# Kernel tuning notes

Hardware: AMD Instinct MI355X
Metric: run time of the kernel (lower is better)

The kernel has to match this reference:

```python
import jax, jax.numpy as jnp
import numpy as np

B, N, D, H = 4, 8192, 1024, 8
HD = D // H  # 128
EPS = 1e-5


def setup_inputs() -> dict:
    key = jax.random.key(0)
    k1, k2, k3 = jax.random.split(key, 3)
    x = jax.random.normal(k1, (B, N, D), dtype=jnp.float32)
    mask = jax.random.randint(k2, (B, 1, N), 0, 2).astype(jnp.bool_)
    # nn.Linear(dim, 3*dim, bias=False): weight [3D, D]; store as [D, 3D] for x @ w
    w_qkv = jax.random.normal(k3, (D, 3 * D), dtype=jnp.float32) / np.sqrt(D)
    gamma = jnp.ones((D,), dtype=jnp.float32)
    beta = jnp.zeros((D,), dtype=jnp.float32)
    return {"x": x, "mask": mask, "w_qkv": w_qkv, "gamma": gamma, "beta": beta}


def _layernorm(x, gamma, beta):
    mu = jnp.mean(x, axis=-1, keepdims=True)
    var = jnp.mean(jnp.square(x - mu), axis=-1, keepdims=True)
    return (x - mu) * jax.lax.rsqrt(var + EPS) * gamma + beta


def reference(x, mask, w_qkv, gamma, beta):
    xn = _layernorm(x, gamma, beta)                       # [B,N,D]
    qkv = xn @ w_qkv                                      # [B,N,3D]
    q, k, v = jnp.split(qkv, 3, axis=-1)
    # 'b n (h d) -> b h n d'
    def to_heads(t):
        return t.reshape(B, N, H, HD).transpose(0, 2, 1, 3)
    q, k, v = to_heads(q), to_heads(k), to_heads(v)       # [B,H,N,HD]
    q = jax.nn.sigmoid(q)
    k = jnp.tanh(k)
    k = jnp.where(mask[..., None], 0.0, k)                # masked_fill -> 0
    kv = jnp.einsum('bhnd,bhne->bhde', k, v)              # k^T @ v, [B,H,HD,HD]
    out = jnp.einsum('bhnd,bhde->bhne', q, kv)            # [B,H,N,HD]
    out = out.transpose(0, 2, 1, 3).reshape(B, N, D)      # 'b h n d -> b n (h d)'
    return out  # output_layer='None' -> Identity
```

## Files before the change

### kernel.cpp

```cpp
#include <hip/hip_runtime.h>

#define EPS 1e-5f
#define B_ 4
#define N_ 8192
#define D_ 1024
#define H_ 8
#define HD_ 128
#define M_TOT 32768
#define NQKV 3072

typedef __bf16 bf16x8 __attribute__((ext_vector_type(8)));
typedef float f32x4 __attribute__((ext_vector_type(4)));

__device__ __forceinline__ float bf2f(unsigned short u) {
    unsigned int v = ((unsigned int)u) << 16;
    return __uint_as_float(v);
}
__device__ __forceinline__ unsigned short f2bf(float f) {
    unsigned int u = __float_as_uint(f);
    u += 0x7fffu + ((u >> 16) & 1u);
    return (unsigned short)(u >> 16);
}

__device__ __forceinline__ float fast_sigmoid(float v) {
    return __builtin_amdgcn_rcpf(1.0f + __expf(-v));
}
__device__ __forceinline__ float fast_tanh(float v) {
    return 1.0f - 2.0f * __builtin_amdgcn_rcpf(1.0f + __expf(2.0f * v));
}

__device__ __forceinline__ void gl_lds16(const void* g, void* l) {
    __builtin_amdgcn_global_load_lds(
        (const __attribute__((address_space(1))) unsigned int*)g,
        (__attribute__((address_space(3))) unsigned int*)l, 16, 0, 0);
}

__global__ __launch_bounds__(256) void ln_kernel(const float* __restrict__ x,
                                                 const float* __restrict__ gamma,
                                                 const float* __restrict__ beta,
                                                 unsigned short* __restrict__ xn) {
    const int row = blockIdx.x;
    const int t = threadIdx.x;
    const float* xr = x + (size_t)row * D_;
    float4 xv = ((const float4*)xr)[t];
    float s = xv.x + xv.y + xv.z + xv.w;
    float s2 = xv.x * xv.x + xv.y * xv.y + xv.z * xv.z + xv.w * xv.w;
    for (int off = 32; off > 0; off >>= 1) {
        s += __shfl_down(s, off);
        s2 += __shfl_down(s2, off);
    }
    __shared__ float red[8];
    if ((t & 63) == 0) { red[t >> 6] = s; red[4 + (t >> 6)] = s2; }
    __syncthreads();
    float ts = red[0] + red[1] + red[2] + red[3];
    float ts2 = red[4] + red[5] + red[6] + red[7];
    float mu = ts * (1.0f / D_);
    float var = ts2 * (1.0f / D_) - mu * mu;
    float rs = rsqrtf(var + EPS);
    float4 g = ((const float4*)gamma)[t];
    float4 bt = ((const float4*)beta)[t];
    ushort4 o;
    o.x = f2bf((xv.x - mu) * rs * g.x + bt.x);
    o.y = f2bf((xv.y - mu) * rs * g.y + bt.y);
    o.z = f2bf((xv.z - mu) * rs * g.z + bt.z);
    o.w = f2bf((xv.w - mu) * rs * g.w + bt.w);
    ((ushort4*)(xn + (size_t)row * D_))[t] = o;
}

__global__ __launch_bounds__(256) void wt_kernel(const float* __restrict__ w,
                                                 unsigned short* __restrict__ wT) {
    __shared__ float tile[64][65];
    const int n0 = blockIdx.x * 64;
    const int k0 = blockIdx.y * 64;
    const int t = threadIdx.x;
    const int tx = t & 63, ty = t >> 6;
    #pragma unroll
    for (int i = 0; i < 16; i++) {
        int r = i * 4 + ty;
        tile[r][tx] = w[(size_t)(k0 + r) * NQKV + n0 + tx];
    }
    __syncthreads();
    #pragma unroll
    for (int i = 0; i < 16; i++) {
        int r = i * 4 + ty;
        wT[(size_t)(n0 + r) * D_ + k0 + tx] = f2bf(tile[tx][r]);
    }
}


#define BAR()   asm volatile("s_barrier" ::: "memory")
#define LGKM0() asm volatile("s_waitcnt lgkmcnt(0)" ::: "memory")
#define VM4()   asm volatile("s_waitcnt vmcnt(4)" ::: "memory")
#define VM0()   asm volatile("s_waitcnt vmcnt(0)" ::: "memory")

#define STAGE(dstTile, srcB, h, ktv) do {                                   \
    const char* s0_ = (srcB) + (size_t)(h) * 262144 + (size_t)(ktv) * 128;  \
    char* d0_ = (dstTile) + (h) * 16384 + w * 1024;                         \
    gl_lds16(s0_, d0_);                                                     \
    gl_lds16(s0_ + 131072, d0_ + 8192);                                     \
} while (0)

#define LDA(Ab, mhv) do {                                                   \
    _Pragma("unroll") for (int i_ = 0; i_ < 4; i_++) {                      \
        const char* rp_ = (Ab) + (size_t)(wm + (mhv) * 64 + i_ * 16 + ln16) * 128; \
        af[i_][0] = *(const bf16x8*)(rp_ + kc0);                            \
        af[i_][1] = *(const bf16x8*)(rp_ + kc1);                            \
    } } while (0)

#define LDB(Bb, nhv) do {                                                   \
    _Pragma("unroll") for (int j_ = 0; j_ < 2; j_++) {                      \
        const char* rp_ = (Bb) + (size_t)(wn + (nhv) * 32 + j_ * 16 + ln16) * 128; \
        bfr[nhv][j_][0] = *(const bf16x8*)(rp_ + kc0);                      \
        bfr[nhv][j_][1] = *(const bf16x8*)(rp_ + kc1);                      \
    } } while (0)

#define MFMAQ(mhv, nhv) do {                                                \
    __builtin_amdgcn_s_setprio(1);                                          \
    _Pragma("unroll") for (int i_ = 0; i_ < 4; i_++)                        \
    _Pragma("unroll") for (int j_ = 0; j_ < 2; j_++) {                      \
        f32x4* ap_ = &acc[(mhv) * 4 + i_][(nhv) * 2 + j_];                  \
        *ap_ = __builtin_amdgcn_mfma_f32_16x16x32_bf16(af[i_][0], bfr[nhv][j_][0], *ap_, 0, 0, 0); \
        *ap_ = __builtin_amdgcn_mfma_f32_16x16x32_bf16(af[i_][1], bfr[nhv][j_][1], *ap_, 0, 0, 0); \
    }                                                                       \
    __builtin_amdgcn_s_setprio(0);                                          \
} while (0)

__global__ __launch_bounds__(512, 2) void qkv_gemm(const unsigned short* __restrict__ xn,
                                                   const unsigned short* __restrict__ wT,
                                                   const int* __restrict__ mask,
                                                   unsigned short* __restrict__ qws,
                                                   unsigned short* __restrict__ kT,
                                                   unsigned short* __restrict__ vT) {
    __shared__ __align__(16) char smem[131072];
    const int t = threadIdx.x;
    const int w = t >> 6, l = t & 63;
    const int quad = l >> 4, ln16 = l & 15;

    const int lin = blockIdx.x;
    const int swz = (lin & 7) * 192 + (lin >> 3);
    const int mt = swz / 12, nt = swz - mt * 12;
    const int m0 = mt * 256, n0 = nt * 256;
    const int wm = (w >> 2) * 128, wn = (w & 3) * 64;

    char* Abuf0 = smem;
    char* Bbuf0 = smem + 32768;
    char* Abuf1 = smem + 65536;
    char* Bbuf1 = smem + 98304;

    const int gsw = (l & 7) ^ (l >> 3);
    const char* aSrc = (const char*)xn + ((size_t)(m0 + w * 8 + (l >> 3)) * 2048) + gsw * 16;
    const char* bSrc = (const char*)wT + ((size_t)(n0 + w * 8 + (l >> 3)) * 2048) + gsw * 16;

    const int r7 = ln16 & 7;
    const int kc0 = ((quad ^ r7) << 4);
    const int kc1 = (((4 | quad) ^ r7) << 4);

    f32x4 acc[8][4] = {};
    bf16x8 af[4][2];
    bf16x8 bfr[2][2][2];

    STAGE(Bbuf0, bSrc, 0, 0); STAGE(Abuf0, aSrc, 0, 0);
    STAGE(Bbuf0, bSrc, 1, 0); STAGE(Abuf0, aSrc, 1, 0);
    STAGE(Bbuf1, bSrc, 0, 1); STAGE(Abuf1, aSrc, 0, 1);
    VM4();
    BAR();

    for (int itn = 0; itn < 8; ++itn) {
        const int ktHi = 2 * itn + 1;
        const int kt2 = 2 * itn + 2, kt3 = 2 * itn + 3;
        const bool pf = (itn < 7);

        LDA(Abuf0, 0); LDB(Bbuf0, 0);
        STAGE(Bbuf1, bSrc, 1, ktHi);
        BAR(); LGKM0(); MFMAQ(0, 0); BAR();

        LDB(Bbuf0, 1);
        STAGE(Abuf1, aSrc, 1, ktHi);
        BAR(); LGKM0(); MFMAQ(0, 1); BAR();

        LDA(Abuf0, 1);
        if (pf) STAGE(Bbuf0, bSrc, 0, kt2);
        BAR(); LGKM0(); MFMAQ(1, 0); BAR();

        if (pf) STAGE(Abuf0, aSrc, 0, kt2);
        BAR(); MFMAQ(1, 1);
        if (pf) { VM4(); } else { VM0(); }
        BAR();

        LDA(Abuf1, 0); LDB(Bbuf1, 0);
        if (pf) STAGE(Bbuf0, bSrc, 1, kt2);
        BAR(); LGKM0(); MFMAQ(0, 0); BAR();

        LDB(Bbuf1, 1);
        if (pf) STAGE(Abuf0, aSrc, 1, kt2);
        BAR(); LGKM0(); MFMAQ(0, 1); BAR();

        LDA(Abuf1, 1);
        if (pf) STAGE(Bbuf1, bSrc, 0, kt3);
        BAR(); LGKM0(); MFMAQ(1, 0); BAR();

        if (pf) STAGE(Abuf1, aSrc, 0, kt3);
        BAR(); MFMAQ(1, 1);
        if (pf) { VM4(); }
        BAR();
    }

    const int region = n0 >> 10;
    const int cbase = n0 & 1023;
    if (region == 0) {
        #pragma unroll
        for (int mi = 0; mi < 8; mi++) {
            #pragma unroll
            for (int r = 0; r < 4; r++) {
                const int gm = m0 + wm + mi * 16 + quad * 4 + r;
                unsigned short* qr = qws + (size_t)gm * D_ + cbase + wn + ln16;
                #pragma unroll
                for (int ni = 0; ni < 4; ni++)
                    qr[ni * 16] = f2bf(fast_sigmoid(acc[mi][ni][r]));
            }
        }
    } else {
        unsigned short* ShT = (unsigned short*)smem;
        unsigned short* dstT = (region == 1) ? kT : vT;
        const int bb = m0 >> 13;
        const int ntok0 = m0 & 8191;
        const int hbase = cbase >> 7;
        #pragma unroll
        for (int pp = 0; pp < 2; pp++) {
            __syncthreads();
            if (((wn >> 7) & 1) == pp) {
                #pragma unroll
                for (int mi = 0; mi < 8; mi++) {
                    const int tok0 = wm + mi * 16 + quad * 4;
                    int mk0 = 0, mk1 = 0, mk2 = 0, mk3 = 0;
                    if (region == 1) {
                        mk0 = mask[m0 + tok0];
                        mk1 = mask[m0 + tok0 + 1];
                        mk2 = mask[m0 + tok0 + 2];
                        mk3 = mask[m0 + tok0 + 3];
                    }
                    #pragma unroll
                    for (int ni = 0; ni < 4; ni++) {
                        const int flp = (wn & 127) + ni * 16 + ln16;
                        float v0 = acc[mi][ni][0], v1 = acc[mi][ni][1];
                        float v2 = acc[mi][ni][2], v3 = acc[mi][ni][3];
                        if (region == 1) {
                            v0 = mk0 ? 0.0f : fast_tanh(v0);
                            v1 = mk1 ? 0.0f : fast_tanh(v1);
                            v2 = mk2 ? 0.0f : fast_tanh(v2);
                            v3 = mk3 ? 0.0f : fast_tanh(v3);
                        }
                        ushort4 pk;
                        pk.x = f2bf(v0); pk.y = f2bf(v1); pk.z = f2bf(v2); pk.w = f2bf(v3);
                        *(ushort4*)&ShT[flp * 264 + tok0] = pk;
                    }
                }
            }
            __syncthreads();
            const int h = hbase + pp;
            unsigned short* dstBase = dstT + ((size_t)(bb * 8 + h) * 128) * 8192 + ntok0;
            #pragma unroll
            for (int itc = 0; itc < 8; itc++) {
                const int idx = itc * 512 + t;
                const int fl = idx >> 5, ch = idx & 31;
                uint4 u = *(const uint4*)&ShT[fl * 264 + ch * 8];
                *(uint4*)(dstBase + (size_t)fl * 8192 + ch * 8) = u;
            }
        }
    }
}

#undef STAGE
#undef LDA
#undef LDB
#undef MFMAQ
#undef BAR
#undef LGKM0
#undef VM4
#undef VM0

__global__ __launch_bounds__(256) void kv_mfma(const unsigned short* __restrict__ kT,
                                               const unsigned short* __restrict__ vT,
                                               float* __restrict__ kv) {
    __shared__ unsigned short As[128 * 32];
    __shared__ unsigned short Bs[128 * 32];
    const int t = threadIdx.x;
    const int w = t >> 6, l = t & 63;
    const int quad = l >> 4, ln16 = l & 15;
    const int bh = blockIdx.y;
    const int kc0 = blockIdx.x * 512;
    const int wm = (w >> 1) * 64, wn = (w & 1) * 64;

    f32x4 acc[4][4] = {};

    const size_t base = (size_t)bh * 128 * 8192;
    const unsigned short* aG = kT + base + (size_t)(w * 16 + (l >> 2)) * 8192
                               + (l & 3) * 8 + kc0;
    const unsigned short* bG = vT + base + (size_t)(w * 16 + (l >> 2)) * 8192
                               + (l & 3) * 8 + kc0;
    char* AsB = (char*)As;
    char* BsB = (char*)Bs;
    char* aL0 = AsB + w * 1024;
    char* aL1 = AsB + 4096 + w * 1024;
    char* bL0 = BsB + w * 1024;
    char* bL1 = BsB + 4096 + w * 1024;

    for (int kk = 0; kk < 512; kk += 32) {
        gl_lds16(aG + kk, aL0);
        gl_lds16(aG + 64 * 8192 + kk, aL1);
        gl_lds16(bG + kk, bL0);
        gl_lds16(bG + 64 * 8192 + kk, bL1);
        __syncthreads();
        bf16x8 af[4], bfr[4];
        #pragma unroll
        for (int mi = 0; mi < 4; mi++)
            af[mi] = *(const bf16x8*)(AsB + (wm + mi * 16 + ln16) * 64 + quad * 16);
        #pragma unroll
        for (int ni = 0; ni < 4; ni++)
            bfr[ni] = *(const bf16x8*)(BsB + (wn + ni * 16 + ln16) * 64 + quad * 16);
        #pragma unroll
        for (int mi = 0; mi < 4; mi++)
            #pragma unroll
            for (int ni = 0; ni < 4; ni++)
                acc[mi][ni] = __builtin_amdgcn_mfma_f32_16x16x32_bf16(af[mi], bfr[ni],
                                                                      acc[mi][ni], 0, 0, 0);
        __syncthreads();
    }

    float* dst = kv + (size_t)bh * (HD_ * HD_);
    #pragma unroll
    for (int mi = 0; mi < 4; mi++) {
        #pragma unroll
        for (int r = 0; r < 4; r++) {
            int d = wm + mi * 16 + quad * 4 + r;
            #pragma unroll
            for (int ni = 0; ni < 4; ni++) {
                int e = wn + ni * 16 + ln16;
                atomicAdd(&dst[d * HD_ + e], acc[mi][ni][r]);
            }
        }
    }
}

__global__ __launch_bounds__(256) void kvcvt(const float* __restrict__ kv,
                                             unsigned short* __restrict__ kvTb) {
    __shared__ float tile[32][132];
    const int bh = blockIdx.x;
    const int c = blockIdx.y;
    const int t = threadIdx.x;
    {
        int r = t >> 3, cc = (t & 7) * 16;
        const float* src = kv + ((size_t)bh * 128 + c * 32 + r) * 128 + cc;
        #pragma unroll
        for (int q4 = 0; q4 < 4; q4++)
            *(float4*)&tile[r][cc + q4 * 4] = *(const float4*)(src + q4 * 4);
    }
    __syncthreads();
    {
        int e = t >> 1, dh = t & 1;
        ushort4 o[4];
        #pragma unroll
        for (int q4 = 0; q4 < 4; q4++) {
            o[q4].x = f2bf(tile[dh * 16 + q4 * 4 + 0][e]);
            o[q4].y = f2bf(tile[dh * 16 + q4 * 4 + 1][e]);
            o[q4].z = f2bf(tile[dh * 16 + q4 * 4 + 2][e]);
            o[q4].w = f2bf(tile[dh * 16 + q4 * 4 + 3][e]);
        }
        unsigned short* dst = kvTb + (size_t)bh * 16384 + e * 128 + c * 32 + dh * 16;
        #pragma unroll
        for (int q4 = 0; q4 < 4; q4++)
            ((ushort4*)dst)[q4] = o[q4];
    }
}

__global__ __launch_bounds__(256) void out_mfma(const unsigned short* __restrict__ qws,
                                                const unsigned short* __restrict__ kvTb,
                                                float* __restrict__ out) {
    __shared__ unsigned short As[128 * 32];
    __shared__ unsigned short Bs[128 * 32];
    const int t = threadIdx.x;
    const int w = t >> 6, l = t & 63;
    const int quad = l >> 4, ln16 = l & 15;
    const int m0 = blockIdx.x * 128;
    const int h = blockIdx.y;
    const int b = m0 >> 13;
    const int bh = b * 8 + h;
    const int wm = (w >> 1) * 64, wn = (w & 1) * 64;

    f32x4 acc[4][4] = {};

    const unsigned short* aG = qws + (size_t)(m0 + w * 16 + (l >> 2)) * D_
                               + h * HD_ + (l & 3) * 8;
    const unsigned short* bG = kvTb + (size_t)bh * 16384
                               + (size_t)(w * 16 + (l >> 2)) * 128 + (l & 3) * 8;
    char* AsB = (char*)As;
    char* BsB = (char*)Bs;

    for (int kk = 0; kk < 128; kk += 32) {
        gl_lds16(aG + kk, AsB + w * 1024);
        gl_lds16(aG + 64 * D_ + kk, AsB + 4096 + w * 1024);
        gl_lds16(bG + kk, BsB + w * 1024);
        gl_lds16(bG + 64 * 128 + kk, BsB + 4096 + w * 1024);
        __syncthreads();
        bf16x8 af[4], bfr[4];
        #pragma unroll
        for (int mi = 0; mi < 4; mi++)
            af[mi] = *(const bf16x8*)(AsB + (wm + mi * 16 + ln16) * 64 + quad * 16);
        #pragma unroll
        for (int ni = 0; ni < 4; ni++)
            bfr[ni] = *(const bf16x8*)(BsB + (wn + ni * 16 + ln16) * 64 + quad * 16);
        #pragma unroll
        for (int mi = 0; mi < 4; mi++)
            #pragma unroll
            for (int ni = 0; ni < 4; ni++)
                acc[mi][ni] = __builtin_amdgcn_mfma_f32_16x16x32_bf16(af[mi], bfr[ni],
                                                                      acc[mi][ni], 0, 0, 0);
        __syncthreads();
    }

    #pragma unroll
    for (int mi = 0; mi < 4; mi++) {
        #pragma unroll
        for (int r = 0; r < 4; r++) {
            int gm = m0 + wm + mi * 16 + quad * 4 + r;
            #pragma unroll
            for (int ni = 0; ni < 4; ni++) {
                int e = wn + ni * 16 + ln16;
                out[(size_t)gm * D_ + h * HD_ + e] = acc[mi][ni][r];
            }
        }
    }
}

extern "C" void kernel_launch(void* const* d_in, const int* in_sizes, int n_in,
                              void* d_out, int out_size, void* d_ws, size_t ws_size,
                              hipStream_t stream) {
    const float* x     = (const float*)d_in[0];
    const int*   mask  = (const int*)d_in[1];
    const float* w     = (const float*)d_in[2];
    const float* gamma = (const float*)d_in[3];
    const float* beta  = (const float*)d_in[4];
    float* out = (float*)d_out;
    char* ws = (char*)d_ws;

    unsigned short* xn  = (unsigned short*)(ws + 0);
    unsigned short* wT  = (unsigned short*)(ws + 67108864ull);
    unsigned short* qws = (unsigned short*)(ws + 73400320ull);
    unsigned short* kT  = (unsigned short*)(ws + 140509184ull);
    unsigned short* vT  = (unsigned short*)(ws + 207618048ull);
    float* kv           = (float*)(ws + 274726912ull);
    unsigned short* kvTb = (unsigned short*)(ws + 276824064ull);

    hipMemsetAsync(kv, 0, 32 * HD_ * HD_ * sizeof(float), stream);
    hipLaunchKernelGGL(ln_kernel, dim3(M_TOT), dim3(256), 0, stream, x, gamma, beta, xn);
    hipLaunchKernelGGL(wt_kernel, dim3(48, 16), dim3(256), 0, stream, w, wT);
    hipLaunchKernelGGL(qkv_gemm, dim3(1536), dim3(512), 0, stream,
                       xn, wT, mask, qws, kT, vT);
    hipLaunchKernelGGL(kv_mfma, dim3(16, 32), dim3(256), 0, stream, kT, vT, kv);
    hipLaunchKernelGGL(kvcvt, dim3(32, 4), dim3(256), 0, stream, kv, kvTb);
    hipLaunchKernelGGL(out_mfma, dim3(M_TOT / 128, 8), dim3(256), 0, stream,
                       qws, kvTb, out);
}
```

Measured before the change: 553.0 us.

## Reschedule QKV GEMM prefetch into whole-tile stages and drop explicit LDS waits

Reorders the global-to-LDS staging in the QKV GEMM main loop. The prologue now preloads both full k-tiles, and each buffer's two halves are issued together, one k-tile ahead, waiting with vmcnt(8) instead of vmcnt(4). The explicit lgkmcnt(0) waits before each MFMA group are removed, so the compiler's own waits on the LDS reads take over. The aim is a deeper, more regular prefetch that lets global loads overlap the MFMA quarters better and cuts redundant waits. The cost is more loads in flight and a reliance on barriers plus compiler-inserted waits to keep LDS reuse safe.

Measured after the change: 563.3 us. About the same (+1.9%).

```diff
diff --git a/kernel.cpp b/kernel.cpp
--- a/kernel.cpp
+++ b/kernel.cpp
@@ -89,8 +89,7 @@
 
 
 #define BAR()   asm volatile("s_barrier" ::: "memory")
-#define LGKM0() asm volatile("s_waitcnt lgkmcnt(0)" ::: "memory")
-#define VM4()   asm volatile("s_waitcnt vmcnt(4)" ::: "memory")
+#define VM8()   asm volatile("s_waitcnt vmcnt(8)" ::: "memory")
 #define VM0()   asm volatile("s_waitcnt vmcnt(0)" ::: "memory")
 
 #define STAGE(dstTile, srcB, h, ktv) do {                                   \
@@ -159,49 +158,45 @@
     bf16x8 af[4][2];
     bf16x8 bfr[2][2][2];
 
-    STAGE(Bbuf0, bSrc, 0, 0); STAGE(Abuf0, aSrc, 0, 0);
-    STAGE(Bbuf0, bSrc, 1, 0); STAGE(Abuf0, aSrc, 1, 0);
-    STAGE(Bbuf1, bSrc, 0, 1); STAGE(Abuf1, aSrc, 0, 1);
-    VM4();
+    STAGE(Bbuf0, bSrc, 0, 0); STAGE(Bbuf0, bSrc, 1, 0);
+    STAGE(Abuf0, aSrc, 0, 0); STAGE(Abuf0, aSrc, 1, 0);
+    STAGE(Bbuf1, bSrc, 0, 1); STAGE(Bbuf1, bSrc, 1, 1);
+    STAGE(Abuf1, aSrc, 0, 1); STAGE(Abuf1, aSrc, 1, 1);
+    VM8();
     BAR();
 
     for (int itn = 0; itn < 8; ++itn) {
-        const int ktHi = 2 * itn + 1;
         const int kt2 = 2 * itn + 2, kt3 = 2 * itn + 3;
         const bool pf = (itn < 7);
 
         LDA(Abuf0, 0); LDB(Bbuf0, 0);
-        STAGE(Bbuf1, bSrc, 1, ktHi);
-        BAR(); LGKM0(); MFMAQ(0, 0); BAR();
+        BAR(); MFMAQ(0, 0); BAR();
 
         LDB(Bbuf0, 1);
-        STAGE(Abuf1, aSrc, 1, ktHi);
-        BAR(); LGKM0(); MFMAQ(0, 1); BAR();
-
+        BAR(); MFMAQ(0, 1); BAR();
+
+        if (pf) { STAGE(Bbuf0, bSrc, 0, kt2); STAGE(Bbuf0, bSrc, 1, kt2); }
         LDA(Abuf0, 1);
-        if (pf) STAGE(Bbuf0, bSrc, 0, kt2);
-        BAR(); LGKM0(); MFMAQ(1, 0); BAR();
-
-        if (pf) STAGE(Abuf0, aSrc, 0, kt2);
+        BAR(); MFMAQ(1, 0); BAR();
+
+        if (pf) { STAGE(Abuf0, aSrc, 0, kt2); STAGE(Abuf0, aSrc, 1, kt2); }
         BAR(); MFMAQ(1, 1);
-        if (pf) { VM4(); } else { VM0(); }
+        if (pf) { VM8(); } else { VM0(); }
         BAR();
 
         LDA(Abuf1, 0); LDB(Bbuf1, 0);
-        if (pf) STAGE(Bbuf0, bSrc, 1, kt2);
-        BAR(); LGKM0(); MFMAQ(0, 0); BAR();
+        BAR(); MFMAQ(0, 0); BAR();
 
         LDB(Bbuf1, 1);
-        if (pf) STAGE(Abuf0, aSrc, 1, kt2);
-        BAR(); LGKM0(); MFMAQ(0, 1); BAR();
-
+        BAR(); MFMAQ(0, 1); BAR();
+
+        if (pf) { STAGE(Bbuf1, bSrc, 0, kt3); STAGE(Bbuf1, bSrc, 1, kt3); }
         LDA(Abuf1, 1);
-        if (pf) STAGE(Bbuf1, bSrc, 0, kt3);
-        BAR(); LGKM0(); MFMAQ(1, 0); BAR();
-
-        if (pf) STAGE(Abuf1, aSrc, 0, kt3);
+        BAR(); MFMAQ(1, 0); BAR();
+
+        if (pf) { STAGE(Abuf1, aSrc, 0, kt3); STAGE(Abuf1, aSrc, 1, kt3); }
         BAR(); MFMAQ(1, 1);
-        if (pf) { VM4(); }
+        if (pf) { VM8(); }
         BAR();
     }
 
@@ -275,8 +270,7 @@
 #undef LDB
 #undef MFMAQ
 #undef BAR
-#undef LGKM0
-#undef VM4
+#undef VM8
 #undef VM0
 
 __global__ __launch_bounds__(256) void kv_mfma(const unsigned short* __restrict__ kT,
```
